# Performance work log

Hardware: AMD Instinct MI355X
Metric: run time of the kernel (lower is better)

Reference implementation:

```python
import jax, jax.numpy as jnp
import numpy as np

CSIZE = 512
KSIZE = 7
BATCH = 4096


def setup_inputs() -> dict:
    key = jax.random.key(0)
    kx, kw, kb = jax.random.split(key, 3)
    x = jax.random.normal(kx, (BATCH, CSIZE, KSIZE, KSIZE), dtype=jnp.float32)
    # per-channel Conv2d(1,1,ksize) weights: one (ksize,ksize) filter + scalar bias per channel
    fan_in = KSIZE * KSIZE  # PyTorch Conv2d kaiming-uniform bound ~ 1/sqrt(fan_in)
    bound = 1.0 / np.sqrt(fan_in)
    W = jax.random.uniform(kw, (CSIZE, KSIZE, KSIZE), minval=-bound, maxval=bound, dtype=jnp.float32)
    b = jax.random.uniform(kb, (CSIZE,), minval=-bound, maxval=bound, dtype=jnp.float32)
    return {"x": x, "W": W, "b": b}


def reference(x, W, b):
    # Each channel i: Conv2d(1,1,ksize) on a ksize x ksize input -> single scalar,
    # i.e. a weighted sum over the spatial plane plus bias, followed by tanh.
    # Fused across all channels as one contraction: [B,C,H,W] x [C,H,W] -> [B,C]
    s = jnp.einsum("bchw,chw->bc", x, W) + b  # (B, C)
    return jnp.tanh(s)
```

## Files before the change

kernel.cpp:

```cpp
#include <hip/hip_runtime.h>
#include <math.h>


constexpr int K    = 49;
constexpr int ROWS = 256;
constexpr int GRID = 2048;

__global__ __launch_bounds__(256) void WGP_84018150245011_kernel(
    const float* __restrict__ x,
    const float* __restrict__ W,
    const float* __restrict__ bias,
    float* __restrict__ out,
    int n_tiles) {
  __shared__ float xs[ROWS * K];

  const int tid = threadIdx.x;

  const int c = ((blockIdx.x & 1) << 8) | tid;

  float w[K];
  const float* __restrict__ wr = W + c * K;
#pragma unroll
  for (int k = 0; k < K; ++k) w[k] = wr[k];
  const float bi = bias[c];

  for (int g = blockIdx.x; g < n_tiles; g += GRID) {
    const float4* __restrict__ src4 =
        reinterpret_cast<const float4*>(x) + (size_t)g * (ROWS * K / 4);
    float4* dst4 = reinterpret_cast<float4*>(xs);
#pragma unroll
    for (int j = 0; j < 12; ++j) {
      dst4[tid + j * 256] = src4[tid + j * 256];
    }
    if (tid < 64) {
      dst4[tid + 3072] = src4[tid + 3072];
    }
    __syncthreads();

    const float* xr = xs + tid * K;
    float s = bi;
#pragma unroll
    for (int k = 0; k < K; ++k) {
      s = fmaf(xr[k], w[k], s);
    }
    out[(size_t)g * ROWS + tid] = tanhf(s);
    __syncthreads();
  }
}

extern "C" void kernel_launch(void* const* d_in, const int* in_sizes, int n_in,
                              void* d_out, int out_size, void* d_ws, size_t ws_size,
                              hipStream_t stream) {
  const float* x    = (const float*)d_in[0];
  const float* W    = (const float*)d_in[1];
  const float* bias = (const float*)d_in[2];
  float* out        = (float*)d_out;

  const int n_rows  = in_sizes[0] / K;
  const int n_tiles = n_rows / ROWS;

  WGP_84018150245011_kernel<<<GRID, ROWS, 0, stream>>>(x, W, bias, out, n_tiles);
}
```

Baseline: 83.35 us.

## Use single-wavefront blocks with register-prefetched next tile, drop barriers

Shrinks each block to one 64-lane wavefront handling 64 rows per tile, and raises the grid to a multiple of 8 so each block keeps a fixed channel slice and its weights in registers. The next tile's global loads are issued into registers before the current tile's dot product and are written to LDS afterwards, overlapping memory latency with compute. Because a block is one wavefront, __syncthreads is replaced by an LDS waitcnt. This trades higher register pressure and more blocks for less barrier stalling and better latency hiding on a bandwidth-bound read.

```diff
diff --git a/kernel.cpp b/kernel.cpp
--- a/kernel.cpp
+++ b/kernel.cpp
@@ -3,20 +3,20 @@
 
 
 constexpr int K    = 49;
-constexpr int ROWS = 256;
-constexpr int GRID = 2048;
+constexpr int TPB  = 64;
+constexpr int GRID = 3328;
 
-__global__ __launch_bounds__(256) void WGP_84018150245011_kernel(
+__global__ __launch_bounds__(64) void WGP_84018150245011_kernel(
     const float* __restrict__ x,
     const float* __restrict__ W,
     const float* __restrict__ bias,
     float* __restrict__ out,
     int n_tiles) {
-  __shared__ float xs[ROWS * K];
+  __shared__ float xs[TPB * K];
 
-  const int tid = threadIdx.x;
+  const int lane = threadIdx.x;
 
-  const int c = ((blockIdx.x & 1) << 8) | tid;
+  const int c = ((blockIdx.x & 7) << 6) | lane;
 
   float w[K];
   const float* __restrict__ wr = W + c * K;
@@ -24,27 +24,53 @@
   for (int k = 0; k < K; ++k) w[k] = wr[k];
   const float bi = bias[c];
 
-  for (int g = blockIdx.x; g < n_tiles; g += GRID) {
+  float4* dst4 = reinterpret_cast<float4*>(xs);
+
+  float4 p[12];
+  float  ptail;
+
+  int t = blockIdx.x;
+
+  {
     const float4* __restrict__ src4 =
-        reinterpret_cast<const float4*>(x) + (size_t)g * (ROWS * K / 4);
-    float4* dst4 = reinterpret_cast<float4*>(xs);
+        reinterpret_cast<const float4*>(x) + (size_t)t * (TPB * K / 4);
 #pragma unroll
-    for (int j = 0; j < 12; ++j) {
-      dst4[tid + j * 256] = src4[tid + j * 256];
+    for (int j = 0; j < 12; ++j) p[j] = src4[lane + j * 64];
+    ptail = x[(size_t)t * (TPB * K) + 3072 + lane];
+#pragma unroll
+    for (int j = 0; j < 12; ++j) dst4[lane + j * 64] = p[j];
+    xs[3072 + lane] = ptail;
+    asm volatile("s_waitcnt lgkmcnt(0)" ::: "memory");
+  }
+
+#pragma unroll 1
+  for (; t < n_tiles;) {
+    const int tn = t + GRID;
+    const bool more = (tn < n_tiles);
+
+    if (more) {
+      const float4* __restrict__ src4 =
+          reinterpret_cast<const float4*>(x) + (size_t)tn * (TPB * K / 4);
+#pragma unroll
+      for (int j = 0; j < 12; ++j) p[j] = src4[lane + j * 64];
+      ptail = x[(size_t)tn * (TPB * K) + 3072 + lane];
     }
-    if (tid < 64) {
-      dst4[tid + 3072] = src4[tid + 3072];
+
+    {
+      const float* xr = xs + lane * K;
+      float s = bi;
+#pragma unroll
+      for (int k = 0; k < K; ++k) s = fmaf(xr[k], w[k], s);
+      out[(size_t)t * TPB + lane] = tanhf(s);
     }
-    __syncthreads();
 
-    const float* xr = xs + tid * K;
-    float s = bi;
+    if (more) {
 #pragma unroll
-    for (int k = 0; k < K; ++k) {
-      s = fmaf(xr[k], w[k], s);
+      for (int j = 0; j < 12; ++j) dst4[lane + j * 64] = p[j];
+      xs[3072 + lane] = ptail;
+      asm volatile("s_waitcnt lgkmcnt(0)" ::: "memory");
     }
-    out[(size_t)g * ROWS + tid] = tanhf(s);
-    __syncthreads();
+    t = tn;
   }
 }
 
@@ -57,7 +83,7 @@
   float* out        = (float*)d_out;
 
   const int n_rows  = in_sizes[0] / K;
-  const int n_tiles = n_rows / ROWS;
+  const int n_tiles = n_rows / TPB;
 
-  WGP_84018150245011_kernel<<<GRID, ROWS, 0, stream>>>(x, W, bias, out, n_tiles);
+  WGP_84018150245011_kernel<<<GRID, TPB, 0, stream>>>(x, W, bias, out, n_tiles);
 }
```

Result: slower. 177.0 us (+112.4%).

## Use single-wave blocks with double-buffered direct global-to-LDS async loads

Applied to the files above, without the earlier changes.

Shrinks each block to one 64-lane wavefront and makes each block own a fixed 64-channel slice. Tiles are staged straight into LDS with global_load_lds, double-buffered so the next tile's load overlaps the current dot product. Waits use explicit vmcnt counters instead of __syncthreads. This relies on exact counts of outstanding loads, assumes the tile count divides evenly by the grid, and makes the kernel issue many more per-lane 16-byte LDS writes.

```diff
diff --git a/kernel.cpp b/kernel.cpp
--- a/kernel.cpp
+++ b/kernel.cpp
@@ -3,20 +3,21 @@
 
 
 constexpr int K    = 49;
-constexpr int ROWS = 256;
+constexpr int TPB  = 64;
+constexpr int TILE = TPB * K;
 constexpr int GRID = 2048;
 
-__global__ __launch_bounds__(256) void WGP_84018150245011_kernel(
+__global__ __launch_bounds__(64) void WGP_84018150245011_kernel(
     const float* __restrict__ x,
     const float* __restrict__ W,
     const float* __restrict__ bias,
     float* __restrict__ out,
-    int n_tiles) {
-  __shared__ float xs[ROWS * K];
+    int iters) {
+  __shared__ float xs[2][TILE];
 
-  const int tid = threadIdx.x;
+  const int lane = threadIdx.x;
 
-  const int c = ((blockIdx.x & 1) << 8) | tid;
+  const int c = ((blockIdx.x & 7) << 6) | lane;
 
   float w[K];
   const float* __restrict__ wr = W + c * K;
@@ -24,28 +25,44 @@
   for (int k = 0; k < K; ++k) w[k] = wr[k];
   const float bi = bias[c];
 
-  for (int g = blockIdx.x; g < n_tiles; g += GRID) {
-    const float4* __restrict__ src4 =
-        reinterpret_cast<const float4*>(x) + (size_t)g * (ROWS * K / 4);
-    float4* dst4 = reinterpret_cast<float4*>(xs);
+  auto stage = [&](int t, int buf) {
+    const float* src = x + (size_t)t * TILE;
 #pragma unroll
     for (int j = 0; j < 12; ++j) {
-      dst4[tid + j * 256] = src4[tid + j * 256];
+      __builtin_amdgcn_global_load_lds(
+          (const __attribute__((address_space(1))) unsigned int*)(src + j * 256 + lane * 4),
+          (__attribute__((address_space(3))) unsigned int*)(&xs[buf][j * 256]),
+          16, 0, 0);
     }
-    if (tid < 64) {
-      dst4[tid + 3072] = src4[tid + 3072];
-    }
-    __syncthreads();
+    __builtin_amdgcn_global_load_lds(
+        (const __attribute__((address_space(1))) unsigned int*)(src + 3072 + lane),
+        (__attribute__((address_space(3))) unsigned int*)(&xs[buf][3072]),
+        4, 0, 0);
+  };
 
-    const float* xr = xs + tid * K;
+  auto compute = [&](int buf, int t) {
+    const float* xr = &xs[buf][lane * K];
     float s = bi;
 #pragma unroll
-    for (int k = 0; k < K; ++k) {
-      s = fmaf(xr[k], w[k], s);
-    }
-    out[(size_t)g * ROWS + tid] = tanhf(s);
-    __syncthreads();
+    for (int k = 0; k < K; ++k) s = fmaf(xr[k], w[k], s);
+    out[(size_t)t * TPB + lane] = tanhf(s);
+  };
+
+  int t   = blockIdx.x;
+  int buf = 0;
+  stage(t, 0);
+
+#pragma unroll 1
+  for (int i = 1; i < iters; ++i) {
+    const int tn = t + GRID;
+    stage(tn, buf ^ 1);
+    asm volatile("s_waitcnt vmcnt(13)" ::: "memory");
+    compute(buf, t);
+    buf ^= 1;
+    t = tn;
   }
+  asm volatile("s_waitcnt vmcnt(0)" ::: "memory");
+  compute(buf, t);
 }
 
 extern "C" void kernel_launch(void* const* d_in, const int* in_sizes, int n_in,
@@ -57,7 +74,8 @@
   float* out        = (float*)d_out;
 
   const int n_rows  = in_sizes[0] / K;
-  const int n_tiles = n_rows / ROWS;
+  const int n_tiles = n_rows / TPB;
+  const int iters   = n_tiles / GRID;
 
-  WGP_84018150245011_kernel<<<GRID, ROWS, 0, stream>>>(x, W, bias, out, n_tiles);
+  WGP_84018150245011_kernel<<<GRID, TPB, 0, stream>>>(x, W, bias, out, iters);
 }
```

New measurement: 84.88 us. About the same (+1.8%).
